# Kernel optimization log

Hardware: AMD Instinct MI355X
Metric: run time of the kernel (lower is better)

## Reference

```python
import jax, jax.numpy as jnp
import numpy as np

N = 50000   # nodes
E = 1600000 # edges
D = 128     # feature dim (in = hidden = 128)


def setup_inputs() -> dict:
    key = jax.random.key(0)
    k1, k2, k3, k4 = jax.random.split(key, 4)
    scale = 1.0 / np.sqrt(D)
    return {
        "x": jax.random.normal(k1, (N, D), jnp.float32),
        "edge_index": jax.random.randint(k2, (2, E), 0, N, dtype=jnp.int32),
        "W0": jax.random.normal(k3, (D, D), jnp.float32) * scale,
        "b0": jnp.zeros((D,), jnp.float32),
        "W1": jax.random.normal(k4, (D, D), jnp.float32) * scale,
        "b1": jnp.zeros((D,), jnp.float32),
    }


def _gcn_norm(edge_index, num_nodes):
    # Add self-loops, compute symmetric normalization D^-1/2 A_hat D^-1/2.
    loop = jnp.arange(num_nodes, dtype=edge_index.dtype)
    src = jnp.concatenate([edge_index[0], loop])
    dst = jnp.concatenate([edge_index[1], loop])
    deg = jax.ops.segment_sum(jnp.ones_like(dst, jnp.float32), dst,
                              num_segments=num_nodes)
    dinv = jnp.where(deg > 0, jax.lax.rsqrt(deg), 0.0)
    norm = dinv[dst] * dinv[src]  # [E+N]
    return src, dst, norm


def _gcn_layer(x, src, dst, norm, W, b, num_nodes):
    h = x @ W                                  # [N, D]
    msg = h[src] * norm[:, None]               # gather + scale  [E+N, D]
    out = jax.ops.segment_sum(msg, dst, num_segments=num_nodes)  # scatter-add
    return out + b


def reference(x, edge_index, W0, b0, W1, b1):
    num_nodes = x.shape[0]
    src, dst, norm = _gcn_norm(edge_index, num_nodes)
    # forward loops over the first k=2 convs, ReLU after each (as in source)
    x = jax.nn.relu(_gcn_layer(x, src, dst, norm, W0, b0, num_nodes))
    x = jax.nn.relu(_gcn_layer(x, src, dst, norm, W1, b1, num_nodes))
    return x
```

## Files before the change

### kernel.cpp

```cpp
#include <hip/hip_runtime.h>
#include <hip/hip_bf16.h>

#define D 128
#define CHUNK 8192


typedef __attribute__((ext_vector_type(8))) short short8;
typedef __attribute__((ext_vector_type(4))) float floatx4;

static __device__ inline unsigned int f2bf(float f) {
    unsigned int u = __float_as_uint(f);
    return (u + 0x7FFFu + ((u >> 16) & 1u)) >> 16;
}
static __device__ inline float4 bf4_to_f4(uint2 p) {
    float4 v;
    v.x = __uint_as_float(p.x << 16);
    v.y = __uint_as_float(p.x & 0xFFFF0000u);
    v.z = __uint_as_float(p.y << 16);
    v.w = __uint_as_float(p.y & 0xFFFF0000u);
    return v;
}

__global__ __launch_bounds__(256) void k0_swizzle(const float* __restrict__ W0,
                                                  const float* __restrict__ W1,
                                                  short8* __restrict__ whi0, short8* __restrict__ wlo0,
                                                  short8* __restrict__ whi1, short8* __restrict__ wlo1) {
    int gid = blockIdx.x * 256 + threadIdx.x;
    const float* W = (gid < 2048) ? W0 : W1;
    short8* whi = (gid < 2048) ? whi0 : whi1;
    short8* wlo = (gid < 2048) ? wlo0 : wlo1;
    int tid = gid & 2047;
    int t = tid >> 8, q = (tid >> 6) & 3, lane = tid & 63;
    short8 hi, lo;
    #pragma unroll
    for (int j = 0; j < 8; ++j) {
        int k = q * 32 + (lane >> 4) * 8 + j;
        int n = t * 16 + (lane & 15);
        float w = W[k * D + n];
        unsigned int h = f2bf(w);
        hi[j] = (short)h;
        lo[j] = (short)f2bf(w - __uint_as_float(h << 16));
    }
    whi[tid] = hi;
    wlo[tid] = lo;
}

__global__ __launch_bounds__(256) void k1_hist(const int* __restrict__ dst,
                                               int* __restrict__ blockhist, int E_) {
    __shared__ int h[256];
    const int b = blockIdx.x, tid = threadIdx.x;
    h[tid] = 0;
    __syncthreads();
    const int e0 = b * CHUNK;
    const int e1 = min(E_, e0 + CHUNK);
    for (int e = e0 + tid; e < e1; e += 256)
        atomicAdd(&h[dst[e] >> 8], 1);
    __syncthreads();
    blockhist[b * 256 + tid] = h[tid];
}

__global__ __launch_bounds__(256) void k2_scan(const int* __restrict__ blockhist,
                                               int* __restrict__ gbase,
                                               int* __restrict__ bucket_offs,
                                               int NB, int NBUK, int E_) {
    __shared__ int s[256];
    const int myb = blockIdx.x, tid = threadIdx.x;
    int total = 0, prefix = 0;
    #pragma unroll 4
    for (int b2 = 0; b2 < NB; ++b2) {
        int t = blockhist[b2 * 256 + tid];
        total += t;
        prefix += (b2 < myb) ? t : 0;
    }
    s[tid] = total;
    __syncthreads();
    #pragma unroll
    for (int off = 1; off < 256; off <<= 1) {
        int x = (tid >= off) ? s[tid - off] : 0;
        __syncthreads();
        s[tid] += x;
        __syncthreads();
    }
    int bstart = s[tid] - total;
    gbase[myb * 256 + tid] = bstart + prefix;
    if (myb == 0) {
        if (tid < NBUK) bucket_offs[tid] = bstart;
        if (tid == 0) bucket_offs[NBUK] = E_;
    }
}

__global__ __launch_bounds__(256) void k3_scatter(const int* __restrict__ dst,
                                                  const int* __restrict__ src,
                                                  const int* __restrict__ gbase,
                                                  unsigned int* __restrict__ buf, int E_) {
    __shared__ int c[256];
    const int b = blockIdx.x, tid = threadIdx.x;
    c[tid] = gbase[b * 256 + tid];
    __syncthreads();
    const int e0 = b * CHUNK;
    const int e1 = min(E_, e0 + CHUNK);
    for (int e = e0 + tid; e < e1; e += 256) {
        int v = dst[e];
        int sdx = src[e];
        int pos = atomicAdd(&c[v >> 8], 1);
        buf[pos] = (unsigned int)sdx | ((unsigned int)(v & 255) << 16);
    }
}

__global__ __launch_bounds__(256) void k4_bucket(const unsigned int* __restrict__ buf,
                                                 const int* __restrict__ bucket_offs,
                                                 int* __restrict__ offs,
                                                 float* __restrict__ dinv,
                                                 int* __restrict__ col, int N_, int E_) {
    __shared__ int h[256];
    __shared__ int s[256];
    __shared__ int c[256];
    const int beta = blockIdx.x, tid = threadIdx.x;
    const int start = bucket_offs[beta];
    const int end   = bucket_offs[beta + 1];

    h[tid] = 0;
    __syncthreads();
    for (int e = start + tid; e < end; e += 256)
        atomicAdd(&h[(buf[e] >> 16) & 255], 1);
    __syncthreads();

    int deg = h[tid];
    s[tid] = deg;
    __syncthreads();
    #pragma unroll
    for (int off = 1; off < 256; off <<= 1) {
        int x = (tid >= off) ? s[tid - off] : 0;
        __syncthreads();
        s[tid] += x;
        __syncthreads();
    }
    int excl = s[tid] - deg;

    int v0 = beta * 256 + tid;
    if (v0 < N_) {
        offs[v0] = start + excl;
        dinv[v0] = rsqrtf((float)(deg + 1));
    }
    if (beta == 0 && tid == 0) offs[N_] = E_;
    c[tid] = start + excl;
    __syncthreads();

    for (int e = start + tid; e < end; e += 256) {
        unsigned int p = buf[e];
        int pos = atomicAdd(&c[(p >> 16) & 255], 1);
        col[pos] = (int)(p & 0xFFFFu);
    }
}

__global__ __launch_bounds__(256) void gemm_mfma(const float* __restrict__ A,
                                                 const short8* __restrict__ whi,
                                                 const short8* __restrict__ wlo,
                                                 const float* __restrict__ dinv,
                                                 uint2* __restrict__ Gb, int nrows) {
    __shared__ float tileT[128][65];

    const int tid  = threadIdx.x;
    const int wave = tid >> 6, lane = tid & 63;
    const int m = lane & 15, quad = lane >> 4;
    const int rowInBlk = wave * 16;
    const int arow = min(blockIdx.x * 64 + rowInBlk + m, nrows - 1);
    const float* Ap = A + (size_t)arow * D + quad * 8;

    floatx4 acc[8];
    #pragma unroll
    for (int t = 0; t < 8; ++t) acc[t] = (floatx4){0.f, 0.f, 0.f, 0.f};

    #pragma unroll
    for (int q = 0; q < 4; ++q) {
        float4 a0 = *(const float4*)(Ap + q * 32);
        float4 a1 = *(const float4*)(Ap + q * 32 + 4);
        float av[8] = {a0.x, a0.y, a0.z, a0.w, a1.x, a1.y, a1.z, a1.w};
        short8 ahi, alo;
        #pragma unroll
        for (int j = 0; j < 8; ++j) {
            unsigned int h = f2bf(av[j]);
            ahi[j] = (short)h;
            alo[j] = (short)f2bf(av[j] - __uint_as_float(h << 16));
        }
        #pragma unroll
        for (int t = 0; t < 8; ++t) {
            short8 bh = whi[(t * 4 + q) * 64 + lane];
            short8 bl = wlo[(t * 4 + q) * 64 + lane];
            acc[t] = __builtin_amdgcn_mfma_f32_16x16x32_bf16(ahi, bh, acc[t], 0, 0, 0);
            acc[t] = __builtin_amdgcn_mfma_f32_16x16x32_bf16(alo, bh, acc[t], 0, 0, 0);
            acc[t] = __builtin_amdgcn_mfma_f32_16x16x32_bf16(ahi, bl, acc[t], 0, 0, 0);
        }
    }

    #pragma unroll
    for (int t = 0; t < 8; ++t)
        #pragma unroll
        for (int r = 0; r < 4; ++r)
            tileT[t * 16 + m][rowInBlk + quad * 4 + r] = acc[t][r];
    __syncthreads();

    const int orow = tid >> 2, seg = tid & 3;
    const int grow = blockIdx.x * 64 + orow;
    if (grow < nrows) {
        float s = dinv[grow];
        #pragma unroll
        for (int i = 0; i < 4; ++i) {
            int c = seg * 32 + i * 8;
            float v0 = tileT[c + 0][orow] * s, v1 = tileT[c + 1][orow] * s;
            float v2 = tileT[c + 2][orow] * s, v3 = tileT[c + 3][orow] * s;
            float v4 = tileT[c + 4][orow] * s, v5 = tileT[c + 5][orow] * s;
            float v6 = tileT[c + 6][orow] * s, v7 = tileT[c + 7][orow] * s;
            uint4 o4;
            o4.x = f2bf(v0) | (f2bf(v1) << 16);
            o4.y = f2bf(v2) | (f2bf(v3) << 16);
            o4.z = f2bf(v4) | (f2bf(v5) << 16);
            o4.w = f2bf(v6) | (f2bf(v7) << 16);
            *(uint4*)&Gb[(size_t)grow * 32 + seg * 8 + i * 2] = o4;
        }
    }
}

__global__ __launch_bounds__(256) void aggregate_kernel(const uint2* __restrict__ Gb,
                                                        const int* __restrict__ offs,
                                                        const int* __restrict__ col,
                                                        const float* __restrict__ dinv,
                                                        const float* __restrict__ bias,
                                                        float* __restrict__ out, int nnodes) {
    const int lane = threadIdx.x & 31;
    const int node = blockIdx.x * 8 + (threadIdx.x >> 5);
    if (node >= nnodes) return;

    float4 acc = bf4_to_f4(Gb[(size_t)node * 32 + lane]);
    int s = offs[node];
    int e = offs[node + 1];

    int idx = s;
    for (; idx + 16 <= e; idx += 16) {
        int j[16];
        #pragma unroll
        for (int u = 0; u < 16; ++u) j[u] = col[idx + u];
        uint2 p[16];
        #pragma unroll
        for (int u = 0; u < 16; ++u) p[u] = Gb[(size_t)j[u] * 32 + lane];
        float4 t0 = make_float4(0.f, 0.f, 0.f, 0.f);
        float4 t1 = make_float4(0.f, 0.f, 0.f, 0.f);
        #pragma unroll
        for (int u = 0; u < 16; u += 2) {
            float4 v0 = bf4_to_f4(p[u]);
            float4 v1 = bf4_to_f4(p[u + 1]);
            t0.x += v0.x; t0.y += v0.y; t0.z += v0.z; t0.w += v0.w;
            t1.x += v1.x; t1.y += v1.y; t1.z += v1.z; t1.w += v1.w;
        }
        acc.x += t0.x + t1.x; acc.y += t0.y + t1.y;
        acc.z += t0.z + t1.z; acc.w += t0.w + t1.w;
    }
    for (; idx + 4 <= e; idx += 4) {
        int j0 = col[idx + 0], j1 = col[idx + 1], j2 = col[idx + 2], j3 = col[idx + 3];
        float4 v0 = bf4_to_f4(Gb[(size_t)j0 * 32 + lane]);
        float4 v1 = bf4_to_f4(Gb[(size_t)j1 * 32 + lane]);
        float4 v2 = bf4_to_f4(Gb[(size_t)j2 * 32 + lane]);
        float4 v3 = bf4_to_f4(Gb[(size_t)j3 * 32 + lane]);
        acc.x += (v0.x + v1.x) + (v2.x + v3.x);
        acc.y += (v0.y + v1.y) + (v2.y + v3.y);
        acc.z += (v0.z + v1.z) + (v2.z + v3.z);
        acc.w += (v0.w + v1.w) + (v2.w + v3.w);
    }
    for (; idx < e; ++idx) {
        float4 v = bf4_to_f4(Gb[(size_t)col[idx] * 32 + lane]);
        acc.x += v.x; acc.y += v.y; acc.z += v.z; acc.w += v.w;
    }

    float dv = dinv[node];
    float4 b = *(const float4*)&bias[lane * 4];
    float4 o;
    o.x = fmaxf(fmaf(dv, acc.x, b.x), 0.f);
    o.y = fmaxf(fmaf(dv, acc.y, b.y), 0.f);
    o.z = fmaxf(fmaf(dv, acc.z, b.z), 0.f);
    o.w = fmaxf(fmaf(dv, acc.w, b.w), 0.f);
    *(float4*)&out[node * D + lane * 4] = o;
}

extern "C" void kernel_launch(void* const* d_in, const int* in_sizes, int n_in,
                              void* d_out, int out_size, void* d_ws, size_t ws_size,
                              hipStream_t stream) {
    const float* x    = (const float*)d_in[0];
    const int*   edge = (const int*)d_in[1];
    const float* W0   = (const float*)d_in[2];
    const float* b0   = (const float*)d_in[3];
    const float* W1   = (const float*)d_in[4];
    const float* b1   = (const float*)d_in[5];
    float* out = (float*)d_out;

    const int N_ = in_sizes[0] / D;
    const int E_ = in_sizes[1] / 2;
    const int* srcp = edge;
    const int* dstp = edge + E_;

    const int NB   = (E_ + CHUNK - 1) / CHUNK;
    const int NBUK = (N_ + 255) >> 8;

    char* p = (char*)d_ws;
    auto carve = [&](size_t bytes) { char* q = p; p += (bytes + 255) & ~(size_t)255; return q; };
    int*          blockhist = (int*)          carve((size_t)NB * 256 * 4);
    int*          gbase     = (int*)          carve((size_t)NB * 256 * 4);
    int*          buck_offs = (int*)          carve((size_t)(NBUK + 1) * 4);
    int*          offs      = (int*)          carve((size_t)(N_ + 1) * 4);
    float*        dinv      = (float*)        carve((size_t)N_ * 4);
    unsigned int* buf       = (unsigned int*) carve((size_t)E_ * 4);
    int*          col       = (int*)          carve((size_t)E_ * 4);
    uint2*        gb        = (uint2*)        carve((size_t)N_ * D * 2);
    short8*       whi0      = (short8*)       carve(2048 * 16);
    short8*       wlo0      = (short8*)       carve(2048 * 16);
    short8*       whi1      = (short8*)       carve(2048 * 16);
    short8*       wlo1      = (short8*)       carve(2048 * 16);

    k0_swizzle<<<16,   256, 0, stream>>>(W0, W1, whi0, wlo0, whi1, wlo1);
    k1_hist   <<<NB,   256, 0, stream>>>(dstp, blockhist, E_);
    k2_scan   <<<NB,   256, 0, stream>>>(blockhist, gbase, buck_offs, NB, NBUK, E_);
    k3_scatter<<<NB,   256, 0, stream>>>(dstp, srcp, gbase, buf, E_);
    k4_bucket <<<NBUK, 256, 0, stream>>>(buf, buck_offs, offs, dinv, col, N_, E_);

    const int gmb = (N_ + 63) / 64;
    const int ab  = (N_ + 7) / 8;

    gemm_mfma       <<<gmb, 256, 0, stream>>>(x, whi0, wlo0, dinv, gb, N_);
    aggregate_kernel<<<ab,  256, 0, stream>>>(gb, offs, col, dinv, b0, out, N_);
    gemm_mfma       <<<gmb, 256, 0, stream>>>(out, whi1, wlo1, dinv, gb, N_);
    aggregate_kernel<<<ab,  256, 0, stream>>>(gb, offs, col, dinv, b1, out, N_);
}
```

Before: 282.7 us.

## Split GEMM output into two feature planes and aggregate per plane; fuse preprocessing

The GEMM now writes its bf16 output as two separate 64-column planes. The aggregation runs a 2-D grid, one plane per blockIdx.y, with each lane gathering 4 bytes instead of 8, so each gathered row segment is 128 bytes. This aims to halve the per-pass gather working set and improve L2 hit rate for the random neighbour gathers, at the cost of reading the col/offs arrays twice and issuing more, smaller loads. Separately, the weight swizzle is fused into the histogram kernel, and the multi-block scan becomes a single-block scan whose bucket offsets are added in the scatter kernel, to cut launch and redundant scan work.

```diff
diff --git a/kernel.cpp b/kernel.cpp
--- a/kernel.cpp
+++ b/kernel.cpp
@@ -12,51 +12,47 @@
     unsigned int u = __float_as_uint(f);
     return (u + 0x7FFFu + ((u >> 16) & 1u)) >> 16;
 }
-static __device__ inline float4 bf4_to_f4(uint2 p) {
-    float4 v;
-    v.x = __uint_as_float(p.x << 16);
-    v.y = __uint_as_float(p.x & 0xFFFF0000u);
-    v.z = __uint_as_float(p.y << 16);
-    v.w = __uint_as_float(p.y & 0xFFFF0000u);
-    return v;
-}
-
-__global__ __launch_bounds__(256) void k0_swizzle(const float* __restrict__ W0,
-                                                  const float* __restrict__ W1,
-                                                  short8* __restrict__ whi0, short8* __restrict__ wlo0,
-                                                  short8* __restrict__ whi1, short8* __restrict__ wlo1) {
-    int gid = blockIdx.x * 256 + threadIdx.x;
-    const float* W = (gid < 2048) ? W0 : W1;
-    short8* whi = (gid < 2048) ? whi0 : whi1;
-    short8* wlo = (gid < 2048) ? wlo0 : wlo1;
-    int tid = gid & 2047;
-    int t = tid >> 8, q = (tid >> 6) & 3, lane = tid & 63;
-    short8 hi, lo;
-    #pragma unroll
-    for (int j = 0; j < 8; ++j) {
-        int k = q * 32 + (lane >> 4) * 8 + j;
-        int n = t * 16 + (lane & 15);
-        float w = W[k * D + n];
-        unsigned int h = f2bf(w);
-        hi[j] = (short)h;
-        lo[j] = (short)f2bf(w - __uint_as_float(h << 16));
-    }
-    whi[tid] = hi;
-    wlo[tid] = lo;
-}
-
-__global__ __launch_bounds__(256) void k1_hist(const int* __restrict__ dst,
-                                               int* __restrict__ blockhist, int E_) {
+static __device__ inline float bflo(unsigned int u) { return __uint_as_float(u << 16); }
+static __device__ inline float bfhi(unsigned int u) { return __uint_as_float(u & 0xFFFF0000u); }
+
+__global__ __launch_bounds__(256) void k01_swz_hist(const float* __restrict__ W0,
+                                                    const float* __restrict__ W1,
+                                                    short8* __restrict__ whi0, short8* __restrict__ wlo0,
+                                                    short8* __restrict__ whi1, short8* __restrict__ wlo1,
+                                                    const int* __restrict__ dst,
+                                                    int* __restrict__ blockhist, int E_) {
     __shared__ int h[256];
-    const int b = blockIdx.x, tid = threadIdx.x;
-    h[tid] = 0;
-    __syncthreads();
-    const int e0 = b * CHUNK;
-    const int e1 = min(E_, e0 + CHUNK);
-    for (int e = e0 + tid; e < e1; e += 256)
-        atomicAdd(&h[dst[e] >> 8], 1);
-    __syncthreads();
-    blockhist[b * 256 + tid] = h[tid];
+    const int tid = threadIdx.x;
+    if (blockIdx.x < 16) {
+        int gid = blockIdx.x * 256 + tid;
+        const float* W = (gid < 2048) ? W0 : W1;
+        short8* whi = (gid < 2048) ? whi0 : whi1;
+        short8* wlo = (gid < 2048) ? wlo0 : wlo1;
+        int t2 = gid & 2047;
+        int t = t2 >> 8, q = (t2 >> 6) & 3, lane = t2 & 63;
+        short8 hi, lo;
+        #pragma unroll
+        for (int j = 0; j < 8; ++j) {
+            int k = q * 32 + (lane >> 4) * 8 + j;
+            int n = t * 16 + (lane & 15);
+            float w = W[k * D + n];
+            unsigned int hh = f2bf(w);
+            hi[j] = (short)hh;
+            lo[j] = (short)f2bf(w - __uint_as_float(hh << 16));
+        }
+        whi[t2] = hi;
+        wlo[t2] = lo;
+    } else {
+        const int b = blockIdx.x - 16;
+        h[tid] = 0;
+        __syncthreads();
+        const int e0 = b * CHUNK;
+        const int e1 = min(E_, e0 + CHUNK);
+        for (int e = e0 + tid; e < e1; e += 256)
+            atomicAdd(&h[dst[e] >> 8], 1);
+        __syncthreads();
+        blockhist[b * 256 + tid] = h[tid];
+    }
 }
 
 __global__ __launch_bounds__(256) void k2_scan(const int* __restrict__ blockhist,
@@ -64,15 +60,14 @@
                                                int* __restrict__ bucket_offs,
                                                int NB, int NBUK, int E_) {
     __shared__ int s[256];
-    const int myb = blockIdx.x, tid = threadIdx.x;
-    int total = 0, prefix = 0;
-    #pragma unroll 4
-    for (int b2 = 0; b2 < NB; ++b2) {
-        int t = blockhist[b2 * 256 + tid];
-        total += t;
-        prefix += (b2 < myb) ? t : 0;
-    }
-    s[tid] = total;
+    const int tid = threadIdx.x;
+    int run = 0;
+    for (int c = 0; c < NB; ++c) {
+        int t = blockhist[c * 256 + tid];
+        gbase[c * 256 + tid] = run;
+        run += t;
+    }
+    s[tid] = run;
     __syncthreads();
     #pragma unroll
     for (int off = 1; off < 256; off <<= 1) {
@@ -81,21 +76,19 @@
         s[tid] += x;
         __syncthreads();
     }
-    int bstart = s[tid] - total;
-    gbase[myb * 256 + tid] = bstart + prefix;
-    if (myb == 0) {
-        if (tid < NBUK) bucket_offs[tid] = bstart;
-        if (tid == 0) bucket_offs[NBUK] = E_;
-    }
+    int excl = s[tid] - run;
+    if (tid < NBUK) bucket_offs[tid] = excl;
+    if (tid == 0) bucket_offs[NBUK] = E_;
 }
 
 __global__ __launch_bounds__(256) void k3_scatter(const int* __restrict__ dst,
                                                   const int* __restrict__ src,
                                                   const int* __restrict__ gbase,
-                                                  unsigned int* __restrict__ buf, int E_) {
+                                                  const int* __restrict__ bucket_offs,
+                                                  unsigned int* __restrict__ buf, int E_, int NBUK) {
     __shared__ int c[256];
     const int b = blockIdx.x, tid = threadIdx.x;
-    c[tid] = gbase[b * 256 + tid];
+    c[tid] = gbase[b * 256 + tid] + ((tid < NBUK) ? bucket_offs[tid] : 0);
     __syncthreads();
     const int e0 = b * CHUNK;
     const int e1 = min(E_, e0 + CHUNK);
@@ -157,7 +150,7 @@
                                                  const short8* __restrict__ whi,
                                                  const short8* __restrict__ wlo,
                                                  const float* __restrict__ dinv,
-                                                 uint2* __restrict__ Gb, int nrows) {
+                                                 unsigned int* __restrict__ Gu, int nrows) {
     __shared__ float tileT[128][65];
 
     const int tid  = threadIdx.x;
@@ -204,81 +197,76 @@
     const int grow = blockIdx.x * 64 + orow;
     if (grow < nrows) {
         float s = dinv[grow];
+        const int p = seg >> 1;
+        unsigned int* Gp = Gu + ((size_t)(p * nrows + grow)) * 32 + (seg & 1) * 16;
         #pragma unroll
         for (int i = 0; i < 4; ++i) {
-            int c = seg * 32 + i * 8;
-            float v0 = tileT[c + 0][orow] * s, v1 = tileT[c + 1][orow] * s;
-            float v2 = tileT[c + 2][orow] * s, v3 = tileT[c + 3][orow] * s;
-            float v4 = tileT[c + 4][orow] * s, v5 = tileT[c + 5][orow] * s;
-            float v6 = tileT[c + 6][orow] * s, v7 = tileT[c + 7][orow] * s;
+            int c0 = seg * 32 + i * 8;
             uint4 o4;
-            o4.x = f2bf(v0) | (f2bf(v1) << 16);
-            o4.y = f2bf(v2) | (f2bf(v3) << 16);
-            o4.z = f2bf(v4) | (f2bf(v5) << 16);
-            o4.w = f2bf(v6) | (f2bf(v7) << 16);
-            *(uint4*)&Gb[(size_t)grow * 32 + seg * 8 + i * 2] = o4;
+            o4.x = f2bf(tileT[c0 + 0][orow] * s) | (f2bf(tileT[c0 + 1][orow] * s) << 16);
+            o4.y = f2bf(tileT[c0 + 2][orow] * s) | (f2bf(tileT[c0 + 3][orow] * s) << 16);
+            o4.z = f2bf(tileT[c0 + 4][orow] * s) | (f2bf(tileT[c0 + 5][orow] * s) << 16);
+            o4.w = f2bf(tileT[c0 + 6][orow] * s) | (f2bf(tileT[c0 + 7][orow] * s) << 16);
+            ((uint4*)Gp)[i] = o4;
         }
     }
 }
 
-__global__ __launch_bounds__(256) void aggregate_kernel(const uint2* __restrict__ Gb,
+__global__ __launch_bounds__(256) void aggregate_kernel(const unsigned int* __restrict__ Gu,
                                                         const int* __restrict__ offs,
                                                         const int* __restrict__ col,
                                                         const float* __restrict__ dinv,
                                                         const float* __restrict__ bias,
                                                         float* __restrict__ out, int nnodes) {
-    const int lane = threadIdx.x & 31;
-    const int node = blockIdx.x * 8 + (threadIdx.x >> 5);
+    const int lane  = threadIdx.x & 31;
+    const int node  = blockIdx.x * 8 + (threadIdx.x >> 5);
+    const int plane = blockIdx.y;
     if (node >= nnodes) return;
-
-    float4 acc = bf4_to_f4(Gb[(size_t)node * 32 + lane]);
+    const unsigned int* P = Gu + (size_t)plane * nnodes * 32;
+
+    unsigned int su = P[(size_t)node * 32 + lane];
+    float ax = bflo(su), ay = bfhi(su);
+
     int s = offs[node];
     int e = offs[node + 1];
-
     int idx = s;
-    for (; idx + 16 <= e; idx += 16) {
-        int j[16];
-        #pragma unroll
-        for (int u = 0; u < 16; ++u) j[u] = col[idx + u];
-        uint2 p[16];
-        #pragma unroll
-        for (int u = 0; u < 16; ++u) p[u] = Gb[(size_t)j[u] * 32 + lane];
-        float4 t0 = make_float4(0.f, 0.f, 0.f, 0.f);
-        float4 t1 = make_float4(0.f, 0.f, 0.f, 0.f);
-        #pragma unroll
-        for (int u = 0; u < 16; u += 2) {
-            float4 v0 = bf4_to_f4(p[u]);
-            float4 v1 = bf4_to_f4(p[u + 1]);
-            t0.x += v0.x; t0.y += v0.y; t0.z += v0.z; t0.w += v0.w;
-            t1.x += v1.x; t1.y += v1.y; t1.z += v1.z; t1.w += v1.w;
-        }
-        acc.x += t0.x + t1.x; acc.y += t0.y + t1.y;
-        acc.z += t0.z + t1.z; acc.w += t0.w + t1.w;
+    for (; idx + 8 <= e; idx += 8) {
+        int j0 = col[idx + 0], j1 = col[idx + 1], j2 = col[idx + 2], j3 = col[idx + 3];
+        int j4 = col[idx + 4], j5 = col[idx + 5], j6 = col[idx + 6], j7 = col[idx + 7];
+        unsigned int u0 = P[(size_t)j0 * 32 + lane];
+        unsigned int u1 = P[(size_t)j1 * 32 + lane];
+        unsigned int u2 = P[(size_t)j2 * 32 + lane];
+        unsigned int u3 = P[(size_t)j3 * 32 + lane];
+        unsigned int u4 = P[(size_t)j4 * 32 + lane];
+        unsigned int u5 = P[(size_t)j5 * 32 + lane];
+        unsigned int u6 = P[(size_t)j6 * 32 + lane];
+        unsigned int u7 = P[(size_t)j7 * 32 + lane];
+        ax += ((bflo(u0) + bflo(u1)) + (bflo(u2) + bflo(u3))) +
+              ((bflo(u4) + bflo(u5)) + (bflo(u6) + bflo(u7)));
+        ay += ((bfhi(u0) + bfhi(u1)) + (bfhi(u2) + bfhi(u3))) +
+              ((bfhi(u4) + bfhi(u5)) + (bfhi(u6) + bfhi(u7)));
     }
     for (; idx + 4 <= e; idx += 4) {
         int j0 = col[idx + 0], j1 = col[idx + 1], j2 = col[idx + 2], j3 = col[idx + 3];
-        float4 v0 = bf4_to_f4(Gb[(size_t)j0 * 32 + lane]);
-        float4 v1 = bf4_to_f4(Gb[(size_t)j1 * 32 + lane]);
-        float4 v2 = bf4_to_f4(Gb[(size_t)j2 * 32 + lane]);
-        float4 v3 = bf4_to_f4(Gb[(size_t)j3 * 32 + lane]);
-        acc.x += (v0.x + v1.x) + (v2.x + v3.x);
-        acc.y += (v0.y + v1.y) + (v2.y + v3.y);
-        acc.z += (v0.z + v1.z) + (v2.z + v3.z);
-        acc.w += (v0.w + v1.w) + (v2.w + v3.w);
+        unsigned int u0 = P[(size_t)j0 * 32 + lane];
+        unsigned int u1 = P[(size_t)j1 * 32 + lane];
+        unsigned int u2 = P[(size_t)j2 * 32 + lane];
+        unsigned int u3 = P[(size_t)j3 * 32 + lane];
+        ax += (bflo(u0) + bflo(u1)) + (bflo(u2) + bflo(u3));
+        ay += (bfhi(u0) + bfhi(u1)) + (bfhi(u2) + bfhi(u3));
     }
     for (; idx < e; ++idx) {
-        float4 v = bf4_to_f4(Gb[(size_t)col[idx] * 32 + lane]);
-        acc.x += v.x; acc.y += v.y; acc.z += v.z; acc.w += v.w;
+        unsigned int u = P[(size_t)col[idx] * 32 + lane];
+        ax += bflo(u);
+        ay += bfhi(u);
     }
 
     float dv = dinv[node];
-    float4 b = *(const float4*)&bias[lane * 4];
-    float4 o;
-    o.x = fmaxf(fmaf(dv, acc.x, b.x), 0.f);
-    o.y = fmaxf(fmaf(dv, acc.y, b.y), 0.f);
-    o.z = fmaxf(fmaf(dv, acc.z, b.z), 0.f);
-    o.w = fmaxf(fmaf(dv, acc.w, b.w), 0.f);
-    *(float4*)&out[node * D + lane * 4] = o;
+    float2 bb = ((const float2*)bias)[plane * 32 + lane];
+    float2 o;
+    o.x = fmaxf(fmaf(dv, ax, bb.x), 0.f);
+    o.y = fmaxf(fmaf(dv, ay, bb.y), 0.f);
+    ((float2*)out)[(size_t)node * 64 + plane * 32 + lane] = o;
 }
 
 extern "C" void kernel_launch(void* const* d_in, const int* in_sizes, int n_in,
@@ -309,23 +297,23 @@
     float*        dinv      = (float*)        carve((size_t)N_ * 4);
     unsigned int* buf       = (unsigned int*) carve((size_t)E_ * 4);
     int*          col       = (int*)          carve((size_t)E_ * 4);
-    uint2*        gb        = (uint2*)        carve((size_t)N_ * D * 2);
+    unsigned int* gu        = (unsigned int*) carve((size_t)N_ * 64 * 4);
     short8*       whi0      = (short8*)       carve(2048 * 16);
     short8*       wlo0      = (short8*)       carve(2048 * 16);
     short8*       whi1      = (short8*)       carve(2048 * 16);
     short8*       wlo1      = (short8*)       carve(2048 * 16);
 
-    k0_swizzle<<<16,   256, 0, stream>>>(W0, W1, whi0, wlo0, whi1, wlo1);
-    k1_hist   <<<NB,   256, 0, stream>>>(dstp, blockhist, E_);
-    k2_scan   <<<NB,   256, 0, stream>>>(blockhist, gbase, buck_offs, NB, NBUK, E_);
-    k3_scatter<<<NB,   256, 0, stream>>>(dstp, srcp, gbase, buf, E_);
-    k4_bucket <<<NBUK, 256, 0, stream>>>(buf, buck_offs, offs, dinv, col, N_, E_);
+    k01_swz_hist<<<16 + NB, 256, 0, stream>>>(W0, W1, whi0, wlo0, whi1, wlo1,
+                                              dstp, blockhist, E_);
+    k2_scan     <<<1,       256, 0, stream>>>(blockhist, gbase, buck_offs, NB, NBUK, E_);
+    k3_scatter  <<<NB,      256, 0, stream>>>(dstp, srcp, gbase, buck_offs, buf, E_, NBUK);
+    k4_bucket   <<<NBUK,    256, 0, stream>>>(buf, buck_offs, offs, dinv, col, N_, E_);
 
     const int gmb = (N_ + 63) / 64;
-    const int ab  = (N_ + 7) / 8;
-
-    gemm_mfma       <<<gmb, 256, 0, stream>>>(x, whi0, wlo0, dinv, gb, N_);
-    aggregate_kernel<<<ab,  256, 0, stream>>>(gb, offs, col, dinv, b0, out, N_);
-    gemm_mfma       <<<gmb, 256, 0, stream>>>(out, whi1, wlo1, dinv, gb, N_);
-    aggregate_kernel<<<ab,  256, 0, stream>>>(gb, offs, col, dinv, b1, out, N_);
-}
+    dim3 ab((N_ + 7) / 8, 2);
+
+    gemm_mfma       <<<gmb, 256, 0, stream>>>(x, whi0, wlo0, dinv, gu, N_);
+    aggregate_kernel<<<ab,  256, 0, stream>>>(gu, offs, col, dinv, b0, out, N_);
+    gemm_mfma       <<<gmb, 256, 0, stream>>>(out, whi1, wlo1, dinv, gu, N_);
+    aggregate_kernel<<<ab,  256, 0, stream>>>(gu, offs, col, dinv, b1, out, N_);
+}
```

Result: slower. 307.1 us (+8.6%).
